# Kernel optimization log

Measured on AMD Instinct MI355X. Metric: run time of the kernel, lower is better.

The kernel has to match this reference:

```python
import jax, jax.numpy as jnp
import numpy as np

GAMMA = 10.0
N_FILTERS = 300
FILTER_SPACING = 0.1


def ssp(x):
    # log(0.5*exp(x) + 0.5) == softplus(x) + log(0.5), numerically stable
    return jax.nn.softplus(x) + jnp.log(0.5)


def setup_inputs() -> dict:
    key = jax.random.key(0)
    ks = jax.random.split(key, 8)
    B, N, NF, H = 4, 256, 128, 128
    node_feat = jax.random.normal(ks[0], (B, N, NF), dtype=jnp.float32)
    pos = jax.random.uniform(ks[1], (B, N, 3), dtype=jnp.float32) * 10.0
    valid = jnp.ones((B, N), dtype=jnp.float32)
    # weights stored [in, out] (torch Linear weight transposed)
    s = 0.05
    W_f1 = jax.random.normal(ks[2], (N_FILTERS, H), dtype=jnp.float32) * s
    W_f2 = jax.random.normal(ks[3], (H, H), dtype=jnp.float32) * s
    W_a1 = jax.random.normal(ks[4], (NF, H), dtype=jnp.float32) * s
    W_a2 = jax.random.normal(ks[5], (H, H), dtype=jnp.float32) * s
    W_a3 = jax.random.normal(ks[6], (H, NF), dtype=jnp.float32) * s
    return {"node_feat": node_feat, "pos": pos, "valid": valid,
            "W_f1": W_f1, "W_f2": W_f2, "W_a1": W_a1, "W_a2": W_a2, "W_a3": W_a3}


def reference(node_feat, pos, valid, W_f1, W_f2, W_a1, W_a2, W_a3):
    # atomwise_linear1
    h = node_feat @ W_a1                                   # [B,N,H]
    # pairwise distances
    vec = pos[:, :, None, :] - pos[:, None, :, :]          # [B,N,N,3]
    dist = jnp.sqrt(jnp.sum(vec * vec, axis=-1))           # [B,N,N]
    # RBF expansion
    centers = jnp.arange(N_FILTERS, dtype=jnp.float32) * FILTER_SPACING
    rbf = jnp.exp(-GAMMA * (dist[..., None] - centers) ** 2)  # [B,N,N,K]
    # filter MLP
    filt = ssp(rbf @ W_f1)                                 # [B,N,N,H]
    filt = ssp(filt @ W_f2)                                # [B,N,N,H]
    # CFConv as written: out[b,i,h] = x[b,i,h] * sum_j filt[b,i,j,h]
    h = h * jnp.sum(filt, axis=2)                          # [B,N,H]
    h = ssp(h @ W_a2)
    h = h @ W_a3                                           # [B,N,NF]
    return node_feat + h * valid[..., None]
```

## Files before the change

### kernel.cpp

```cpp
#include <hip/hip_runtime.h>


typedef _Float16 f16x8 __attribute__((ext_vector_type(8)));
typedef _Float16 f16x2 __attribute__((ext_vector_type(2)));
typedef float f32x4 __attribute__((ext_vector_type(4)));

__device__ __forceinline__ float exp2f_fast(float x) {
#if __has_builtin(__builtin_amdgcn_exp2f)
  return __builtin_amdgcn_exp2f(x);
#else
  return __exp2f(x);
#endif
}
__device__ __forceinline__ float log2f_fast(float x) {
#if __has_builtin(__builtin_amdgcn_logf)
  return __builtin_amdgcn_logf(x);
#else
  return __log2f(x);
#endif
}

__device__ __forceinline__ float ssp_l2p(float a) {
  return log2f_fast(fmaf(0.5f, exp2f_fast(a), 0.5f));
}
__device__ __forceinline__ float ssp_l2(float x) {
  return ssp_l2p(1.44269504f * x);
}

__device__ __forceinline__ f16x2 pk2(float a, float b) {
#if __has_builtin(__builtin_amdgcn_cvt_pkrtz)
  return __builtin_bit_cast(f16x2, __builtin_amdgcn_cvt_pkrtz(a, b));
#else
  f16x2 t;
  t.x = (_Float16)a;
  t.y = (_Float16)b;
  return t;
#endif
}

__device__ __forceinline__ f16x8 rbf8(float dd, int kk, int lq) {
  const float x0 = dd - 0.1f * (float)(kk * 32 + lq * 8);
  float v = exp2f_fast(-14.4269504f * x0 * x0);
  float r = exp2f_fast(fmaf(2.88539008f, x0, -0.144269504f));
  float w0 = v;
  v *= r; r *= 0.818730753f; float w1 = v;
  v *= r; r *= 0.818730753f; float w2 = v;
  v *= r; r *= 0.818730753f; float w3 = v;
  v *= r; r *= 0.818730753f; float w4 = v;
  v *= r; r *= 0.818730753f; float w5 = v;
  v *= r; r *= 0.818730753f; float w6 = v;
  v *= r;                    float w7 = v;
  union { f16x8 v8; f16x2 p[4]; } u;
  u.p[0] = pk2(w0, w1);
  u.p[1] = pk2(w2, w3);
  u.p[2] = pk2(w4, w5);
  u.p[3] = pk2(w6, w7);
  return u.v8;
}

__global__ void prep_pack(const float* __restrict__ W1, const float* __restrict__ W2,
                          unsigned short* __restrict__ ws) {
  int gid = blockIdx.x * 256 + threadIdx.x;
  if (gid < 40960) {
    int j = gid & 7, l = (gid >> 3) & 63, ntg = (gid >> 9) & 7, kk = gid >> 12;
    int k = kk * 32 + (l >> 4) * 8 + j;
    int h = ntg * 16 + (l & 15);
    float v = (k < 300) ? 1.44269504f * W1[k * 128 + h] : 0.f;
    ws[gid] = __builtin_bit_cast(unsigned short, (_Float16)v);
  } else if (gid < 57344) {
    int g2 = gid - 40960;
    int j = g2 & 7, l = (g2 >> 3) & 63, ntg = (g2 >> 9) & 7, kk = g2 >> 12;
    int k = kk * 32 + (l >> 4) * 8 + j;
    int h = ntg * 16 + (l & 15);
    ws[gid] = __builtin_bit_cast(unsigned short, (_Float16)W2[k * 128 + h]);
  }
}

__global__ __launch_bounds__(512, 4) void interaction_kernel(
    const float* __restrict__ nodef, const float* __restrict__ pos,
    const float* __restrict__ valid, const unsigned short* __restrict__ ws,
    const float* __restrict__ Wa1, const float* __restrict__ Wa2,
    const float* __restrict__ Wa3, float* __restrict__ out) {
  __shared__ __align__(16) _Float16 ytile[2][64 * 136];
  __shared__ __align__(16) unsigned short W2pk[16384];
  __shared__ float d_lds[256];
  __shared__ int k0arr[256];
  __shared__ unsigned short jord[256];
  __shared__ unsigned short pr[2][256];
  __shared__ int kklo[16], kkhi[16];
  __shared__ float xrow[128], h1row[128], hhrow[128], a2row[128];
  __shared__ float partial[4][128];

  const int t = threadIdx.x;
  const int bid = blockIdx.x;
  const int b = bid >> 8;

  {
    const uint4* src = (const uint4*)(ws + 40960);
    uint4* d2 = (uint4*)W2pk;
    for (int i = t; i < 2048; i += 512) d2[i] = src[i];
  }
  if (t < 128) xrow[t] = nodef[bid * 128 + t];
  if (t < 256) {
    const float qx = pos[bid * 3 + 0], qy = pos[bid * 3 + 1], qz = pos[bid * 3 + 2];
    const float px = pos[(b * 256 + t) * 3 + 0];
    const float py = pos[(b * 256 + t) * 3 + 1];
    const float pz = pos[(b * 256 + t) * 3 + 2];
    const float dx = px - qx, dy = py - qy, dz = pz - qz;
    const float dd = sqrtf(dx * dx + dy * dy + dz * dz);
    d_lds[t] = dd;
    k0arr[t] = __float2int_rn(dd * 10.f);
  }
  __syncthreads();

  {
    const int j = t & 255, half = t >> 8;
    const int key = k0arr[j];
    int rank = 0;
    const int base = half * 128;
    for (int j2 = base; j2 < base + 128; ++j2) {
      const int k2 = k0arr[j2];
      rank += (k2 < key || (k2 == key && j2 < j)) ? 1 : 0;
    }
    pr[half][j] = (unsigned short)rank;
  }
  {
    const int hh_ = t & 127, part = t >> 7;
    float a = 0.f;
#pragma unroll 8
    for (int k = part * 32; k < part * 32 + 32; ++k) a += xrow[k] * Wa1[k * 128 + hh_];
    partial[part][hh_] = a;
  }
  __syncthreads();
  if (t < 256) jord[pr[0][t] + pr[1][t]] = (unsigned short)t;
  if (t < 128)
    h1row[t] = partial[0][t] + partial[1][t] + partial[2][t] + partial[3][t];
  __syncthreads();
  if (t < 16) {
    const int base = t * 16;
    const int klo = max(0, k0arr[jord[base]] - 12);
    const int khi = min(319, k0arr[jord[base + 15]] + 12);
    kklo[t] = klo >> 5;
    kkhi[t] = (khi >> 5) + 1;
  }
  __syncthreads();

  const int wid = t >> 6, l = t & 63;
  const int jg = wid >> 1, hgrp = wid & 1;
  const int lr = l & 15, lq = l >> 4;
  float sumv[4] = {0.f, 0.f, 0.f, 0.f};
  f32x4 acc[4];
  f32x4 acc2[4];

  for (int cc = 0; cc < 4; ++cc) {
    const int buf = cc & 1;
    const int g = cc * 4 + jg;
    const float dd = d_lds[jord[cc * 64 + jg * 16 + lr]];
    const int lo = kklo[g];
    const int n = kkhi[g] - lo;

#pragma unroll
    for (int r = 0; r < 4; ++r) acc[r] = f32x4{0, 0, 0, 0};
    const unsigned short* pb = &ws[((lo * 8 + hgrp * 4) * 64 + l) * 8];
    const f16x8 c00 = *(const f16x8*)(pb + 0 * 512);
    const f16x8 c01 = *(const f16x8*)(pb + 1 * 512);
    const f16x8 c02 = *(const f16x8*)(pb + 2 * 512);
    const f16x8 c03 = *(const f16x8*)(pb + 3 * 512);
    f16x8 c10, c11, c12, c13;
    if (n > 1) {
      c10 = *(const f16x8*)(pb + 4096 + 0 * 512);
      c11 = *(const f16x8*)(pb + 4096 + 1 * 512);
      c12 = *(const f16x8*)(pb + 4096 + 2 * 512);
      c13 = *(const f16x8*)(pb + 4096 + 3 * 512);
    }
    {
      const f16x8 af0 = rbf8(dd, lo, lq);
      acc[0] = __builtin_amdgcn_mfma_f32_16x16x32_f16(af0, c00, acc[0], 0, 0, 0);
      acc[1] = __builtin_amdgcn_mfma_f32_16x16x32_f16(af0, c01, acc[1], 0, 0, 0);
      acc[2] = __builtin_amdgcn_mfma_f32_16x16x32_f16(af0, c02, acc[2], 0, 0, 0);
      acc[3] = __builtin_amdgcn_mfma_f32_16x16x32_f16(af0, c03, acc[3], 0, 0, 0);
    }
    if (n > 1) {
      const f16x8 af1 = rbf8(dd, lo + 1, lq);
      acc[0] = __builtin_amdgcn_mfma_f32_16x16x32_f16(af1, c10, acc[0], 0, 0, 0);
      acc[1] = __builtin_amdgcn_mfma_f32_16x16x32_f16(af1, c11, acc[1], 0, 0, 0);
      acc[2] = __builtin_amdgcn_mfma_f32_16x16x32_f16(af1, c12, acc[2], 0, 0, 0);
      acc[3] = __builtin_amdgcn_mfma_f32_16x16x32_f16(af1, c13, acc[3], 0, 0, 0);
    }
    for (int kk = lo + 2; kk < lo + n; ++kk) {
      const unsigned short* p = pb + (kk - lo) * 4096;
      const f16x8 d0 = *(const f16x8*)(p + 0 * 512);
      const f16x8 d1 = *(const f16x8*)(p + 1 * 512);
      const f16x8 d2 = *(const f16x8*)(p + 2 * 512);
      const f16x8 d3 = *(const f16x8*)(p + 3 * 512);
      const f16x8 af = rbf8(dd, kk, lq);
      acc[0] = __builtin_amdgcn_mfma_f32_16x16x32_f16(af, d0, acc[0], 0, 0, 0);
      acc[1] = __builtin_amdgcn_mfma_f32_16x16x32_f16(af, d1, acc[1], 0, 0, 0);
      acc[2] = __builtin_amdgcn_mfma_f32_16x16x32_f16(af, d2, acc[2], 0, 0, 0);
      acc[3] = __builtin_amdgcn_mfma_f32_16x16x32_f16(af, d3, acc[3], 0, 0, 0);
    }
#pragma unroll
    for (int nt = 0; nt < 4; ++nt)
#pragma unroll
      for (int r = 0; r < 4; ++r)
        ytile[buf][(jg * 16 + lq * 4 + r) * 136 + hgrp * 64 + nt * 16 + lr] =
            (_Float16)ssp_l2p(acc[nt][r]);
    __syncthreads();

#pragma unroll
    for (int r = 0; r < 4; ++r) acc2[r] = f32x4{0, 0, 0, 0};
#pragma unroll
    for (int kk = 0; kk < 4; ++kk) {
      const f16x8 afr =
          *(const f16x8*)&ytile[buf][(jg * 16 + lr) * 136 + kk * 32 + lq * 8];
#pragma unroll
      for (int nt = 0; nt < 4; ++nt) {
        const f16x8 bfr = *(const f16x8*)&W2pk[((kk * 8 + hgrp * 4 + nt) * 64 + l) * 8];
        acc2[nt] = __builtin_amdgcn_mfma_f32_16x16x32_f16(afr, bfr, acc2[nt], 0, 0, 0);
      }
    }
#pragma unroll
    for (int nt = 0; nt < 4; ++nt)
#pragma unroll
      for (int r = 0; r < 4; ++r) sumv[nt] += ssp_l2p(acc2[nt][r]);
  }

  {
    float* red = (float*)&ytile[0][0];
#pragma unroll
    for (int nt = 0; nt < 4; ++nt)
      red[(jg * 4 + lq) * 128 + hgrp * 64 + nt * 16 + lr] = 0.69314718f * sumv[nt];
  }
  __syncthreads();
  if (t < 128) {
    const float* red = (const float*)&ytile[0][0];
    float s = 0.f;
#pragma unroll
    for (int q = 0; q < 16; ++q) s += red[q * 128 + t];
    hhrow[t] = h1row[t] * s;
  }
  __syncthreads();
  {
    const int hh_ = t & 127, part = t >> 7;
    float a = 0.f;
#pragma unroll 32
    for (int k = part * 32; k < part * 32 + 32; ++k) a += hhrow[k] * Wa2[k * 128 + hh_];
    partial[part][hh_] = a;
  }
  __syncthreads();
  if (t < 128)
    a2row[t] = 0.69314718f *
               ssp_l2(partial[0][t] + partial[1][t] + partial[2][t] + partial[3][t]);
  __syncthreads();
  {
    const int hh_ = t & 127, part = t >> 7;
    float a = 0.f;
#pragma unroll 32
    for (int k = part * 32; k < part * 32 + 32; ++k) a += a2row[k] * Wa3[k * 128 + hh_];
    partial[part][hh_] = a;
  }
  __syncthreads();
  if (t < 128)
    out[bid * 128 + t] =
        xrow[t] + (partial[0][t] + partial[1][t] + partial[2][t] + partial[3][t]) * valid[bid];
}

extern "C" void kernel_launch(void* const* d_in, const int* in_sizes, int n_in,
                              void* d_out, int out_size, void* d_ws, size_t ws_size,
                              hipStream_t stream) {
  const float* nodef = (const float*)d_in[0];
  const float* pos   = (const float*)d_in[1];
  const float* valid = (const float*)d_in[2];
  const float* W1    = (const float*)d_in[3];
  const float* W2    = (const float*)d_in[4];
  const float* Wa1   = (const float*)d_in[5];
  const float* Wa2   = (const float*)d_in[6];
  const float* Wa3   = (const float*)d_in[7];
  float* outp = (float*)d_out;
  unsigned short* wsp = (unsigned short*)d_ws;

  prep_pack<<<224, 256, 0, stream>>>(W1, W2, wsp);
  interaction_kernel<<<1024, 512, 0, stream>>>(nodef, pos, valid, wsp,
                                               Wa1, Wa2, Wa3, outp);
}
```

Before: 49.34 us.

## Give each wave a full j-group across both H halves to drop per-chunk barriers

Work is re-partitioned so each of the 8 waves owns 16 pair rows and computes both 64-wide H halves of the first filter layer itself. It then runs the second filter GEMM on its own ytile rows, so no cross-wave data exchange or __syncthreads is needed inside the loop. The chunk loop drops from 4 iterations to 2, and the double-buffered ytile becomes one larger private-per-wave region. In exchange, each wave recomputes the RBF fragments for both halves and carries 8 partial sums, so register pressure rises and the final reduction reads 32 rows instead of 16.

```diff
diff --git a/kernel.cpp b/kernel.cpp
--- a/kernel.cpp
+++ b/kernel.cpp
@@ -81,7 +81,7 @@
     const float* __restrict__ valid, const unsigned short* __restrict__ ws,
     const float* __restrict__ Wa1, const float* __restrict__ Wa2,
     const float* __restrict__ Wa3, float* __restrict__ out) {
-  __shared__ __align__(16) _Float16 ytile[2][64 * 136];
+  __shared__ __align__(16) _Float16 ytile[128 * 136];
   __shared__ __align__(16) unsigned short W2pk[16384];
   __shared__ float d_lds[256];
   __shared__ int k0arr[256];
@@ -145,98 +145,106 @@
   }
   __syncthreads();
 
-  const int wid = t >> 6, l = t & 63;
-  const int jg = wid >> 1, hgrp = wid & 1;
+  const int w = t >> 6, l = t & 63;
   const int lr = l & 15, lq = l >> 4;
-  float sumv[4] = {0.f, 0.f, 0.f, 0.f};
+  float sumv[8];
+#pragma unroll
+  for (int r = 0; r < 8; ++r) sumv[r] = 0.f;
   f32x4 acc[4];
-  f32x4 acc2[4];
-
-  for (int cc = 0; cc < 4; ++cc) {
-    const int buf = cc & 1;
-    const int g = cc * 4 + jg;
-    const float dd = d_lds[jord[cc * 64 + jg * 16 + lr]];
+
+  for (int it = 0; it < 2; ++it) {
+    const int g = it * 8 + w;
+    const float dd = d_lds[jord[it * 128 + w * 16 + lr]];
     const int lo = kklo[g];
     const int n = kkhi[g] - lo;
 
 #pragma unroll
-    for (int r = 0; r < 4; ++r) acc[r] = f32x4{0, 0, 0, 0};
-    const unsigned short* pb = &ws[((lo * 8 + hgrp * 4) * 64 + l) * 8];
-    const f16x8 c00 = *(const f16x8*)(pb + 0 * 512);
-    const f16x8 c01 = *(const f16x8*)(pb + 1 * 512);
-    const f16x8 c02 = *(const f16x8*)(pb + 2 * 512);
-    const f16x8 c03 = *(const f16x8*)(pb + 3 * 512);
-    f16x8 c10, c11, c12, c13;
-    if (n > 1) {
-      c10 = *(const f16x8*)(pb + 4096 + 0 * 512);
-      c11 = *(const f16x8*)(pb + 4096 + 1 * 512);
-      c12 = *(const f16x8*)(pb + 4096 + 2 * 512);
-      c13 = *(const f16x8*)(pb + 4096 + 3 * 512);
-    }
-    {
-      const f16x8 af0 = rbf8(dd, lo, lq);
-      acc[0] = __builtin_amdgcn_mfma_f32_16x16x32_f16(af0, c00, acc[0], 0, 0, 0);
-      acc[1] = __builtin_amdgcn_mfma_f32_16x16x32_f16(af0, c01, acc[1], 0, 0, 0);
-      acc[2] = __builtin_amdgcn_mfma_f32_16x16x32_f16(af0, c02, acc[2], 0, 0, 0);
-      acc[3] = __builtin_amdgcn_mfma_f32_16x16x32_f16(af0, c03, acc[3], 0, 0, 0);
-    }
-    if (n > 1) {
-      const f16x8 af1 = rbf8(dd, lo + 1, lq);
-      acc[0] = __builtin_amdgcn_mfma_f32_16x16x32_f16(af1, c10, acc[0], 0, 0, 0);
-      acc[1] = __builtin_amdgcn_mfma_f32_16x16x32_f16(af1, c11, acc[1], 0, 0, 0);
-      acc[2] = __builtin_amdgcn_mfma_f32_16x16x32_f16(af1, c12, acc[2], 0, 0, 0);
-      acc[3] = __builtin_amdgcn_mfma_f32_16x16x32_f16(af1, c13, acc[3], 0, 0, 0);
-    }
-    for (int kk = lo + 2; kk < lo + n; ++kk) {
-      const unsigned short* p = pb + (kk - lo) * 4096;
-      const f16x8 d0 = *(const f16x8*)(p + 0 * 512);
-      const f16x8 d1 = *(const f16x8*)(p + 1 * 512);
-      const f16x8 d2 = *(const f16x8*)(p + 2 * 512);
-      const f16x8 d3 = *(const f16x8*)(p + 3 * 512);
-      const f16x8 af = rbf8(dd, kk, lq);
-      acc[0] = __builtin_amdgcn_mfma_f32_16x16x32_f16(af, d0, acc[0], 0, 0, 0);
-      acc[1] = __builtin_amdgcn_mfma_f32_16x16x32_f16(af, d1, acc[1], 0, 0, 0);
-      acc[2] = __builtin_amdgcn_mfma_f32_16x16x32_f16(af, d2, acc[2], 0, 0, 0);
-      acc[3] = __builtin_amdgcn_mfma_f32_16x16x32_f16(af, d3, acc[3], 0, 0, 0);
-    }
-#pragma unroll
-    for (int nt = 0; nt < 4; ++nt)
-#pragma unroll
-      for (int r = 0; r < 4; ++r)
-        ytile[buf][(jg * 16 + lq * 4 + r) * 136 + hgrp * 64 + nt * 16 + lr] =
-            (_Float16)ssp_l2p(acc[nt][r]);
-    __syncthreads();
-
-#pragma unroll
-    for (int r = 0; r < 4; ++r) acc2[r] = f32x4{0, 0, 0, 0};
-#pragma unroll
-    for (int kk = 0; kk < 4; ++kk) {
-      const f16x8 afr =
-          *(const f16x8*)&ytile[buf][(jg * 16 + lr) * 136 + kk * 32 + lq * 8];
-#pragma unroll
-      for (int nt = 0; nt < 4; ++nt) {
-        const f16x8 bfr = *(const f16x8*)&W2pk[((kk * 8 + hgrp * 4 + nt) * 64 + l) * 8];
-        acc2[nt] = __builtin_amdgcn_mfma_f32_16x16x32_f16(afr, bfr, acc2[nt], 0, 0, 0);
-      }
-    }
-#pragma unroll
-    for (int nt = 0; nt < 4; ++nt)
-#pragma unroll
-      for (int r = 0; r < 4; ++r) sumv[nt] += ssp_l2p(acc2[nt][r]);
-  }
-
-  {
-    float* red = (float*)&ytile[0][0];
-#pragma unroll
-    for (int nt = 0; nt < 4; ++nt)
-      red[(jg * 4 + lq) * 128 + hgrp * 64 + nt * 16 + lr] = 0.69314718f * sumv[nt];
+    for (int hg = 0; hg < 2; ++hg) {
+#pragma unroll
+      for (int r = 0; r < 4; ++r) acc[r] = f32x4{0, 0, 0, 0};
+      const unsigned short* pb = &ws[((lo * 8 + hg * 4) * 64 + l) * 8];
+      const f16x8 c00 = *(const f16x8*)(pb + 0 * 512);
+      const f16x8 c01 = *(const f16x8*)(pb + 1 * 512);
+      const f16x8 c02 = *(const f16x8*)(pb + 2 * 512);
+      const f16x8 c03 = *(const f16x8*)(pb + 3 * 512);
+      f16x8 c10, c11, c12, c13;
+      if (n > 1) {
+        c10 = *(const f16x8*)(pb + 4096 + 0 * 512);
+        c11 = *(const f16x8*)(pb + 4096 + 1 * 512);
+        c12 = *(const f16x8*)(pb + 4096 + 2 * 512);
+        c13 = *(const f16x8*)(pb + 4096 + 3 * 512);
+      }
+      {
+        const f16x8 af0 = rbf8(dd, lo, lq);
+        acc[0] = __builtin_amdgcn_mfma_f32_16x16x32_f16(af0, c00, acc[0], 0, 0, 0);
+        acc[1] = __builtin_amdgcn_mfma_f32_16x16x32_f16(af0, c01, acc[1], 0, 0, 0);
+        acc[2] = __builtin_amdgcn_mfma_f32_16x16x32_f16(af0, c02, acc[2], 0, 0, 0);
+        acc[3] = __builtin_amdgcn_mfma_f32_16x16x32_f16(af0, c03, acc[3], 0, 0, 0);
+      }
+      if (n > 1) {
+        const f16x8 af1 = rbf8(dd, lo + 1, lq);
+        acc[0] = __builtin_amdgcn_mfma_f32_16x16x32_f16(af1, c10, acc[0], 0, 0, 0);
+        acc[1] = __builtin_amdgcn_mfma_f32_16x16x32_f16(af1, c11, acc[1], 0, 0, 0);
+        acc[2] = __builtin_amdgcn_mfma_f32_16x16x32_f16(af1, c12, acc[2], 0, 0, 0);
+        acc[3] = __builtin_amdgcn_mfma_f32_16x16x32_f16(af1, c13, acc[3], 0, 0, 0);
+      }
+      for (int kk = lo + 2; kk < lo + n; ++kk) {
+        const unsigned short* p = pb + (kk - lo) * 4096;
+        const f16x8 d0 = *(const f16x8*)(p + 0 * 512);
+        const f16x8 d1 = *(const f16x8*)(p + 1 * 512);
+        const f16x8 d2 = *(const f16x8*)(p + 2 * 512);
+        const f16x8 d3 = *(const f16x8*)(p + 3 * 512);
+        const f16x8 af = rbf8(dd, kk, lq);
+        acc[0] = __builtin_amdgcn_mfma_f32_16x16x32_f16(af, d0, acc[0], 0, 0, 0);
+        acc[1] = __builtin_amdgcn_mfma_f32_16x16x32_f16(af, d1, acc[1], 0, 0, 0);
+        acc[2] = __builtin_amdgcn_mfma_f32_16x16x32_f16(af, d2, acc[2], 0, 0, 0);
+        acc[3] = __builtin_amdgcn_mfma_f32_16x16x32_f16(af, d3, acc[3], 0, 0, 0);
+      }
+#pragma unroll
+      for (int nt = 0; nt < 4; ++nt)
+#pragma unroll
+        for (int r = 0; r < 4; ++r)
+          ytile[(w * 16 + lq * 4 + r) * 136 + hg * 64 + nt * 16 + lr] =
+              (_Float16)ssp_l2p(acc[nt][r]);
+    }
+
+#pragma unroll
+    for (int hg2 = 0; hg2 < 2; ++hg2) {
+#pragma unroll
+      for (int r = 0; r < 4; ++r) acc[r] = f32x4{0, 0, 0, 0};
+#pragma unroll
+      for (int kk = 0; kk < 4; ++kk) {
+        const f16x8 afr =
+            *(const f16x8*)&ytile[(w * 16 + lr) * 136 + kk * 32 + lq * 8];
+#pragma unroll
+        for (int nt = 0; nt < 4; ++nt) {
+          const f16x8 bfr =
+              *(const f16x8*)&W2pk[((kk * 8 + hg2 * 4 + nt) * 64 + l) * 8];
+          acc[nt] = __builtin_amdgcn_mfma_f32_16x16x32_f16(afr, bfr, acc[nt], 0, 0, 0);
+        }
+      }
+#pragma unroll
+      for (int nt = 0; nt < 4; ++nt)
+#pragma unroll
+        for (int r = 0; r < 4; ++r) sumv[hg2 * 4 + nt] += ssp_l2p(acc[nt][r]);
+    }
+  }
+
+  __syncthreads();
+  {
+    float* red = (float*)&ytile[0];
+#pragma unroll
+    for (int q = 0; q < 8; ++q) {
+      const int hg2 = q >> 2, nt = q & 3;
+      red[(w * 4 + lq) * 128 + hg2 * 64 + nt * 16 + lr] = 0.69314718f * sumv[q];
+    }
   }
   __syncthreads();
   if (t < 128) {
-    const float* red = (const float*)&ytile[0][0];
+    const float* red = (const float*)&ytile[0];
     float s = 0.f;
 #pragma unroll
-    for (int q = 0; q < 16; ++q) s += red[q * 128 + t];
+    for (int q = 0; q < 32; ++q) s += red[q * 128 + t];
     hhrow[t] = h1row[t] * s;
   }
   __syncthreads();
```

New measurement: 46.89 us. 1.05x faster.
